# Kernel optimization log

Hardware: AMD Instinct MI355X
Metric: run time of the kernel (lower is better)

The kernel has to match this reference:

```python
import jax, jax.numpy as jnp
import numpy as np

C_M, C_Z, H, C_HID = 256, 128, 8, 32
N_SEQ, N_RES = 64, 384
INF = 1e9
EPS = 1e-5


def layernorm(x, w, b):
    mu = jnp.mean(x, axis=-1, keepdims=True)
    var = jnp.mean(jnp.square(x - mu), axis=-1, keepdims=True)
    return (x - mu) * jax.lax.rsqrt(var + EPS) * w + b


def setup_inputs() -> dict:
    key = jax.random.key(0)
    ks = jax.random.split(key, 6)
    m = jax.random.normal(ks[0], (N_SEQ, N_RES, C_M), dtype=jnp.float32)
    z = jax.random.normal(ks[1], (N_RES, N_RES, C_Z), dtype=jnp.float32)
    mask = jnp.ones((N_SEQ, N_RES), dtype=jnp.float32)
    return {
        "m": m,
        "z": z,
        "mask": mask,
        "ln_m_w": jnp.ones((C_M,), jnp.float32),
        "ln_m_b": jnp.zeros((C_M,), jnp.float32),
        "ln_z_w": jnp.ones((C_Z,), jnp.float32),
        "ln_z_b": jnp.zeros((C_Z,), jnp.float32),
        "W_z": jax.random.normal(ks[2], (C_Z, H), jnp.float32) * 0.05,
        "W_v": jax.random.normal(ks[3], (C_M, H * C_HID), jnp.float32) * 0.05,
        "W_g": jax.random.normal(ks[4], (C_M, H * C_HID), jnp.float32) * 0.05,
        "W_o": jax.random.normal(ks[5], (H * C_HID, C_M), jnp.float32) * 0.05,
    }


def reference(m, z, mask, ln_m_w, ln_m_b, ln_z_w, ln_z_b, W_z, W_v, W_g, W_o):
    S, N = m.shape[0], m.shape[1]
    # mask: max over MSA rows, keepdim -> [1, N]; bias -> [1,1,1,N]
    mask_max = jnp.max(mask, axis=-2, keepdims=True)
    mask_bias = (INF * (mask_max - 1.0))[:, None, None, :]  # [1,1,1,N]
    # pair bias: LN(z) @ W_z -> [N,N,H] -> [H,N,N]
    zb = layernorm(z, ln_z_w, ln_z_b) @ W_z  # [N,N,H]
    zb = jnp.transpose(zb, (2, 0, 1))  # [H,N,N]
    # LN on m
    m_ln = layernorm(m, ln_m_w, ln_m_b)  # [S,N,C_m]
    # values: [S,N,H*c] -> [S,H,N,c]
    v = (m_ln @ W_v).reshape(S, N, H, C_HID).transpose(0, 2, 1, 3)
    # attention weights from summed biases (no QK): [1,H,N,N] after broadcast
    a = jax.nn.softmax(mask_bias + zb[None], axis=-1)  # [1,H,N,N]
    # o = a @ v  -> [S,H,N,c]
    o = jnp.einsum('hqk,shkc->shqc', a[0], v)
    o = o.transpose(0, 2, 1, 3)  # [S,N,H,c]
    # sigmoid gate
    g = jax.nn.sigmoid(m_ln @ W_g).reshape(S, N, H, C_HID)
    o = (o * g).reshape(S, N, H * C_HID)
    return o @ W_o  # [S,N,C_m]
```

## Files before the change

### kernel.cpp

```cpp
#include <hip/hip_runtime.h>
#include <math.h>

#define S 64
#define NRES 384
#define CM 256
#define CZ 128
#define NH 8
#define CH 32
#define HC 256
#define NROW 147456

typedef unsigned short u16;
typedef __attribute__((ext_vector_type(8))) short bf16x8;
typedef __attribute__((ext_vector_type(4))) float f32x4;
typedef __attribute__((ext_vector_type(8))) unsigned short ushort8;
typedef __attribute__((ext_vector_type(4))) unsigned short ushort4_t;

#define OFF_BIAS 0
#define OFF_WWT  8192
#define OFF_C1   16384
#define OFF_C2   16448
#define OFF_WT   200704
#define OFF_WOT  462848
#define OFF_A    593920
#define OFF_VT   2953216
#define OFF_G    15536128
#define OFF_O    28119040
#define OFF_MLN  40701952
#define OFF_ZB   OFF_O

__device__ __forceinline__ u16 f2bf(float f) {
    union { float f; unsigned int u; } v; v.f = f;
    unsigned int u = v.u;
    u += 0x7fff + ((u >> 16) & 1);
    return (u16)(u >> 16);
}
__device__ __forceinline__ float bf2f(u16 b) {
    union { float f; unsigned int u; } v; v.u = ((unsigned int)b) << 16;
    return v.f;
}
__device__ __forceinline__ void gload16(const u16* g, u16* l) {
    __builtin_amdgcn_global_load_lds(
        (const __attribute__((address_space(1))) void*)g,
        (__attribute__((address_space(3))) void*)l, 16, 0, 0);
}

__global__ __launch_bounds__(256) void k_pre(
        const float* __restrict__ mask, const float* __restrict__ Wz,
        const float* __restrict__ lzw, const float* __restrict__ lzb,
        const float* __restrict__ Wv, const float* __restrict__ Wg,
        const float* __restrict__ Wo, const float* __restrict__ m,
        const float* __restrict__ lmw, const float* __restrict__ lmb,
        float* __restrict__ bias, u16* __restrict__ WWT,
        float* __restrict__ C1, float* __restrict__ C2,
        u16* __restrict__ Wt, u16* __restrict__ Wot, u16* __restrict__ mln) {
    __shared__ float sRed[4][64];
    const int bid = blockIdx.x, tid = threadIdx.x;
    const int wave = tid >> 6, lane = tid & 63;
    if (bid < 6) {
        const int k = bid * 64 + lane;
        float mx = -1e30f;
        #pragma unroll
        for (int i = 0; i < 16; ++i) {
            const int s = wave * 16 + i;
            mx = fmaxf(mx, mask[(size_t)s * NRES + k]);
        }
        sRed[wave][lane] = mx;
        __syncthreads();
        if (wave == 0) {
            mx = fmaxf(fmaxf(sRed[0][lane], sRed[1][lane]),
                       fmaxf(sRed[2][lane], sRed[3][lane]));
            bias[k] = 1e9f * (mx - 1.0f);
        }
    } else if (bid == 6) {
        __shared__ float sP[2][2][8];
        if (tid < 128) {
            const int c = tid;
            const float4 wz0 = *(const float4*)&Wz[c * 8];
            const float4 wz1 = *(const float4*)&Wz[c * 8 + 4];
            const float lw = lzw[c], lbv = lzb[c];
            float wzv[8] = {wz0.x, wz0.y, wz0.z, wz0.w, wz1.x, wz1.y, wz1.z, wz1.w};
            float ww[8], wb[8];
            #pragma unroll
            for (int h = 0; h < 8; ++h) {
                ww[h] = lw * wzv[h];
                wb[h] = lbv * wzv[h];
                WWT[h * 128 + c] = f2bf(ww[h]);
                WWT[(8 + h) * 128 + c] = 0;
            }
            #pragma unroll
            for (int h = 0; h < 8; ++h) {
                #pragma unroll
                for (int off = 1; off < 64; off <<= 1) {
                    ww[h] += __shfl_xor(ww[h], off);
                    wb[h] += __shfl_xor(wb[h], off);
                }
            }
            if (lane == 0) {
                #pragma unroll
                for (int h = 0; h < 8; ++h) {
                    sP[wave][0][h] = ww[h];
                    sP[wave][1][h] = wb[h];
                }
            }
        }
        __syncthreads();
        if (tid < 8) {
            C1[tid] = sP[0][0][tid] + sP[1][0][tid];
            C2[tid] = sP[0][1][tid] + sP[1][1][tid];
        }
    } else if (bid < 519) {
        const int i = (bid - 7) * 256 + tid;
        const int n = i >> 8, k = i & 255;
        const float v = (n < HC) ? Wv[(size_t)k * HC + n] : Wg[(size_t)k * HC + (n - HC)];
        Wt[i] = f2bf(v);
    } else if (bid < 775) {
        const int i = (bid - 519) * 256 + tid;
        const int n = i >> 8, k = i & 255;
        Wot[i] = f2bf(Wo[(size_t)k * CM + n]);
    } else {
        const int row = (bid - 775) * 4 + wave;
        const float4 x = *(const float4*)&m[(size_t)row * CM + lane * 4];
        float sm = x.x + x.y + x.z + x.w;
        float sq = x.x*x.x + x.y*x.y + x.z*x.z + x.w*x.w;
        #pragma unroll
        for (int off = 32; off >= 1; off >>= 1) {
            sm += __shfl_xor(sm, off);
            sq += __shfl_xor(sq, off);
        }
        const float mu = sm * (1.0f / CM);
        const float var = sq * (1.0f / CM) - mu * mu;
        const float rs = rsqrtf(var + 1e-5f);
        const float4 w4 = *(const float4*)&lmw[lane * 4];
        const float4 b4 = *(const float4*)&lmb[lane * 4];
        u16 t4[4];
        t4[0] = f2bf((x.x - mu) * rs * w4.x + b4.x);
        t4[1] = f2bf((x.y - mu) * rs * w4.y + b4.y);
        t4[2] = f2bf((x.z - mu) * rs * w4.z + b4.z);
        t4[3] = f2bf((x.w - mu) * rs * w4.w + b4.w);
        *(ushort4_t*)&mln[(size_t)row * CM + lane * 4] = *(ushort4_t*)t4;
    }
}

__global__ __launch_bounds__(256) void k_zb(
        const float* __restrict__ z, const u16* __restrict__ WWT,
        const float* __restrict__ C1, const float* __restrict__ C2,
        float* __restrict__ zb) {
    __shared__ u16 sZ[4][2048];
    __shared__ float sSt[4][2][16];
    const int tid = threadIdx.x, wave = tid >> 6, lane = tid & 63;
    const int rl = lane & 15, kg = lane >> 4;
    u16* myZ = &sZ[wave][0];
    const int row0 = blockIdx.x * 64 + wave * 16;
    const float4* zbase = (const float4*)(z + (size_t)row0 * CZ);
    float4 xb[8];
    #pragma unroll
    for (int j = 0; j < 8; ++j) xb[j] = zbase[lane + 64 * j];
    bf16x8 bfr[4];
    #pragma unroll
    for (int t = 0; t < 4; ++t)
        bfr[t] = *(const bf16x8*)&WWT[rl * 128 + t * 32 + kg * 8];
    const float c1 = (rl < 8) ? C1[rl] : 0.f;
    const float c2 = (rl < 8) ? C2[rl] : 0.f;
    const int hw = lane >> 5, c4 = lane & 31;
    float smj[8], sqj[8];
    #pragma unroll
    for (int j = 0; j < 8; ++j) {
        const int r = 2 * j + hw;
        const float4 x = xb[j];
        float xs[4] = {x.x, x.y, x.z, x.w};
        float sm = 0.f, sq = 0.f;
        u16 t4[4];
        #pragma unroll
        for (int e = 0; e < 4; ++e) {
            sm += xs[e]; sq += xs[e] * xs[e];
            t4[e] = f2bf(xs[e]);
        }
        smj[j] = sm; sqj[j] = sq;
        *(ushort4_t*)&myZ[r * 128 + ((c4 >> 1) ^ (r & 7)) * 8 + (c4 & 1) * 4] =
            *(ushort4_t*)t4;
    }
    #pragma unroll
    for (int j = 0; j < 8; ++j) {
        #pragma unroll
        for (int off = 1; off < 32; off <<= 1) {
            smj[j] += __shfl_xor(smj[j], off);
            sqj[j] += __shfl_xor(sqj[j], off);
        }
    }
    if ((lane & 31) == 0) {
        #pragma unroll
        for (int j = 0; j < 8; ++j) {
            const int r = 2 * j + hw;
            const float mu = smj[j] * (1.0f / CZ);
            const float var = sqj[j] * (1.0f / CZ) - mu * mu;
            sSt[wave][0][r] = mu;
            sSt[wave][1][r] = rsqrtf(var + 1e-5f);
        }
    }
    bf16x8 af[4];
    #pragma unroll
    for (int t = 0; t < 4; ++t)
        af[t] = *(const bf16x8*)&myZ[rl * 128 + ((t * 4 + kg) ^ (rl & 7)) * 8];
    f32x4 acc = {};
    #pragma unroll
    for (int t = 0; t < 4; ++t)
        acc = __builtin_amdgcn_mfma_f32_16x16x32_bf16(af[t], bfr[t], acc, 0, 0, 0);
    f32x4 pv;
    #pragma unroll
    for (int r = 0; r < 4; ++r) {
        const int rr = kg * 4 + r;
        pv[r] = sSt[wave][1][rr] * (acc[r] - sSt[wave][0][rr] * c1) + c2;
    }
    if (rl < 8)
        *(f32x4*)&zb[(size_t)rl * NROW + row0 + kg * 4] = pv;
}

__global__ __launch_bounds__(256) void k_stage2(
        const u16* __restrict__ mln, const u16* __restrict__ Wt,
        const float* __restrict__ zb, const float* __restrict__ bias,
        u16* __restrict__ vt, u16* __restrict__ g_, u16* __restrict__ a_out) {
    __shared__ u16 As[128][32];
    __shared__ u16 Bs[128][32];
    const int bid = blockIdx.x, tid = threadIdx.x;
    if (bid >= 768) {
        const int w = (bid - 768) * 4 + (tid >> 6);
        const int lane = tid & 63;
        const int h = w & 7, q = w >> 3;
        const float* zbh = zb + (size_t)h * NROW + (size_t)q * NRES;
        float v[6];
        float mx = -1e30f;
        #pragma unroll
        for (int t = 0; t < 6; ++t) {
            const int k = lane + 64 * t;
            v[t] = zbh[k] + bias[k];
            mx = fmaxf(mx, v[t]);
        }
        #pragma unroll
        for (int off = 32; off >= 1; off >>= 1) mx = fmaxf(mx, __shfl_xor(mx, off));
        float sum = 0.f;
        #pragma unroll
        for (int t = 0; t < 6; ++t) { v[t] = expf(v[t] - mx); sum += v[t]; }
        #pragma unroll
        for (int off = 32; off >= 1; off >>= 1) sum += __shfl_xor(sum, off);
        const float inv = 1.0f / sum;
        #pragma unroll
        for (int t = 0; t < 6; ++t)
            a_out[((size_t)h * NRES + q) * NRES + lane + 64 * t] = f2bf(v[t] * inv);
        return;
    }
    const int xcd = bid & 7, idx = bid >> 3;
    const int nt = idx & 3, mt = xcd * 24 + (idx >> 2);
    const int m0 = mt * 128, n0 = nt * 128;
    const int wave = tid >> 6, lane = tid & 63;
    const int wm = (wave >> 1) * 64, wn = (wave & 1) * 64;
    const int rl = lane & 15, kg = lane >> 4;
    const int lr = lane >> 2, lk = (lane & 3) * 8;
    const int wr = wave * 32;
    const u16* ag  = mln + (size_t)(m0 + wr + lr) * CM + lk;
    const u16* ag2 = ag + 16 * CM;
    const u16* bg  = Wt + (size_t)(n0 + wr + lr) * CM + lk;
    const u16* bg2 = bg + 16 * CM;
    u16* al  = &As[wr][0];
    u16* al2 = &As[wr + 16][0];
    u16* bl  = &Bs[wr][0];
    u16* bl2 = &Bs[wr + 16][0];
    const bool vhalf = (n0 < HC);
    f32x4 acc[4][4] = {};
    for (int kt = 0; kt < CM; kt += 32) {
        if (kt) __syncthreads();
        gload16(ag + kt, al);  gload16(ag2 + kt, al2);
        gload16(bg + kt, bl);  gload16(bg2 + kt, bl2);
        __syncthreads();
        bf16x8 af[4], bfr[4];
        #pragma unroll
        for (int i = 0; i < 4; ++i) af[i]  = *(const bf16x8*)&As[wm + i*16 + rl][kg*8];
        #pragma unroll
        for (int j = 0; j < 4; ++j) bfr[j] = *(const bf16x8*)&Bs[wn + j*16 + rl][kg*8];
        if (vhalf) {
            #pragma unroll
            for (int j = 0; j < 4; ++j)
                #pragma unroll
                for (int i = 0; i < 4; ++i)
                    acc[j][i] = __builtin_amdgcn_mfma_f32_16x16x32_bf16(bfr[j], af[i], acc[j][i], 0, 0, 0);
        } else {
            #pragma unroll
            for (int i = 0; i < 4; ++i)
                #pragma unroll
                for (int j = 0; j < 4; ++j)
                    acc[i][j] = __builtin_amdgcn_mfma_f32_16x16x32_bf16(af[i], bfr[j], acc[i][j], 0, 0, 0);
        }
    }
    if (vhalf) {
        #pragma unroll
        for (int j = 0; j < 4; ++j)
            #pragma unroll
            for (int r = 0; r < 4; ++r) {
                const int vcol = n0 + wn + j*16 + kg*4 + r;
                const int h = vcol >> 5, c = vcol & 31;
                #pragma unroll
                for (int i = 0; i < 4; ++i) {
                    const int mrowb = m0 + wm + i*16;
                    const int s = mrowb / NRES;
                    const int nn = mrowb - s * NRES + rl;
                    vt[(((size_t)h * S + s) * CH + c) * NRES + nn] = f2bf(acc[j][i][r]);
                }
            }
    } else {
        #pragma unroll
        for (int i = 0; i < 4; ++i)
            #pragma unroll
            for (int r = 0; r < 4; ++r) {
                const int row = m0 + wm + i*16 + kg*4 + r;
                #pragma unroll
                for (int j = 0; j < 4; ++j) {
                    const int gc = n0 + wn + j*16 + rl - HC;
                    g_[(size_t)row * HC + gc] = f2bf(1.0f / (1.0f + expf(-acc[i][j][r])));
                }
            }
    }
}

__global__ __launch_bounds__(256) void k_attn2(const u16* __restrict__ a_,
        const u16* __restrict__ vt, u16* __restrict__ o_) {
    __shared__ u16 As[128][32];
    __shared__ u16 Bs[128][32];
    const int tid = threadIdx.x;
    const int h = blockIdx.x & 7, rem = blockIdx.x >> 3;
    const int mt = rem >> 4, nt = rem & 15;
    const int q0 = mt * 128, sc0 = nt * 128;
    const int wave = tid >> 6, lane = tid & 63;
    const int wm = (wave >> 1) * 64, wn = (wave & 1) * 64;
    const int rl = lane & 15, kg = lane >> 4;
    const int lr = lane >> 2, lk = (lane & 3) * 8;
    const int wr = wave * 32;
    const u16* ag  = a_ + (size_t)h * NRES * NRES + (size_t)(q0 + wr + lr) * NRES + lk;
    const u16* ag2 = ag + 16 * NRES;
    const u16* bg  = vt + (size_t)h * S * CH * NRES + (size_t)(sc0 + wr + lr) * NRES + lk;
    const u16* bg2 = bg + 16 * NRES;
    u16* al  = &As[wr][0];
    u16* al2 = &As[wr + 16][0];
    u16* bl  = &Bs[wr][0];
    u16* bl2 = &Bs[wr + 16][0];
    f32x4 acc[4][4] = {};
    for (int kt = 0; kt < NRES; kt += 32) {
        if (kt) __syncthreads();
        gload16(ag + kt, al);  gload16(ag2 + kt, al2);
        gload16(bg + kt, bl);  gload16(bg2 + kt, bl2);
        __syncthreads();
        bf16x8 af[4], bfr[4];
        #pragma unroll
        for (int i = 0; i < 4; ++i) af[i]  = *(const bf16x8*)&As[wm + i*16 + rl][kg*8];
        #pragma unroll
        for (int j = 0; j < 4; ++j) bfr[j] = *(const bf16x8*)&Bs[wn + j*16 + rl][kg*8];
        #pragma unroll
        for (int i = 0; i < 4; ++i)
            #pragma unroll
            for (int j = 0; j < 4; ++j)
                acc[i][j] = __builtin_amdgcn_mfma_f32_16x16x32_bf16(af[i], bfr[j], acc[i][j], 0, 0, 0);
    }
    #pragma unroll
    for (int i = 0; i < 4; ++i)
        #pragma unroll
        for (int r = 0; r < 4; ++r) {
            const int q = q0 + wm + i*16 + kg*4 + r;
            #pragma unroll
            for (int j = 0; j < 4; ++j) {
                const int sc = sc0 + wn + j*16 + rl;
                const int s = sc >> 5, c = sc & 31;
                o_[(((size_t)s * NRES + q) * NH + h) * CH + c] = f2bf(acc[i][j][r]);
            }
        }
}

__global__ __launch_bounds__(256) void k_gemm_out(const u16* __restrict__ o_,
        const u16* __restrict__ g_, const u16* __restrict__ Wot,
        float* __restrict__ out) {
    __shared__ u16 As[128][40];
    __shared__ u16 Bs[128][32];
    const int tid = threadIdx.x;
    const int xcd = blockIdx.x & 7, idx = blockIdx.x >> 3;
    const int nt = idx & 1, mt = xcd * 24 + (idx >> 1);
    const int m0 = mt * 128, n0 = nt * 128;
    const int wave = tid >> 6, lane = tid & 63;
    const int wm = (wave >> 1) * 64, wn = (wave & 1) * 64;
    const int rl = lane & 15, kg = lane >> 4;
    const int lr = lane >> 2, lk = (lane & 3) * 8;
    const int wr = wave * 32;
    const int sr = tid >> 1, sh = (tid & 1) * 16;
    const u16* orow = o_ + (size_t)(m0 + sr) * HC;
    const u16* grow = g_ + (size_t)(m0 + sr) * HC;
    const u16* bg  = Wot + (size_t)(n0 + wr + lr) * HC + lk;
    const u16* bg2 = bg + 16 * HC;
    u16* bl  = &Bs[wr][0];
    u16* bl2 = &Bs[wr + 16][0];
    f32x4 acc[4][4] = {};
    for (int kt = 0; kt < HC; kt += 32) {
        if (kt) __syncthreads();
        gload16(bg + kt, bl);  gload16(bg2 + kt, bl2);
        {
            u16 tmp[16];
            const ushort8 ov0 = *(const ushort8*)&orow[kt + sh];
            const ushort8 ov1 = *(const ushort8*)&orow[kt + sh + 8];
            const ushort8 gv0 = *(const ushort8*)&grow[kt + sh];
            const ushort8 gv1 = *(const ushort8*)&grow[kt + sh + 8];
            #pragma unroll
            for (int p = 0; p < 8; ++p) {
                tmp[p]     = f2bf(bf2f(ov0[p]) * bf2f(gv0[p]));
                tmp[p + 8] = f2bf(bf2f(ov1[p]) * bf2f(gv1[p]));
            }
            *(ushort8*)&As[sr][sh]     = *(ushort8*)&tmp[0];
            *(ushort8*)&As[sr][sh + 8] = *(ushort8*)&tmp[8];
        }
        __syncthreads();
        bf16x8 af[4], bfr[4];
        #pragma unroll
        for (int i = 0; i < 4; ++i) af[i]  = *(const bf16x8*)&As[wm + i*16 + rl][kg*8];
        #pragma unroll
        for (int j = 0; j < 4; ++j) bfr[j] = *(const bf16x8*)&Bs[wn + j*16 + rl][kg*8];
        #pragma unroll
        for (int i = 0; i < 4; ++i)
            #pragma unroll
            for (int j = 0; j < 4; ++j)
                acc[i][j] = __builtin_amdgcn_mfma_f32_16x16x32_bf16(af[i], bfr[j], acc[i][j], 0, 0, 0);
    }
    #pragma unroll
    for (int i = 0; i < 4; ++i)
        #pragma unroll
        for (int r = 0; r < 4; ++r) {
            const int row = m0 + wm + i*16 + kg*4 + r;
            #pragma unroll
            for (int j = 0; j < 4; ++j)
                out[(size_t)row * CM + n0 + wn + j*16 + rl] = acc[i][j][r];
        }
}

extern "C" void kernel_launch(void* const* d_in, const int* in_sizes, int n_in,
                              void* d_out, int out_size, void* d_ws, size_t ws_size,
                              hipStream_t stream) {
    const float* m      = (const float*)d_in[0];
    const float* z      = (const float*)d_in[1];
    const float* mask   = (const float*)d_in[2];
    const float* ln_m_w = (const float*)d_in[3];
    const float* ln_m_b = (const float*)d_in[4];
    const float* ln_z_w = (const float*)d_in[5];
    const float* ln_z_b = (const float*)d_in[6];
    const float* Wz     = (const float*)d_in[7];
    const float* Wv     = (const float*)d_in[8];
    const float* Wg     = (const float*)d_in[9];
    const float* Wo     = (const float*)d_in[10];
    float* out = (float*)d_out;
    char* ws = (char*)d_ws;

    float* bias = (float*)(ws + OFF_BIAS);
    u16* WWT    = (u16*)(ws + OFF_WWT);
    float* C1   = (float*)(ws + OFF_C1);
    float* C2   = (float*)(ws + OFF_C2);
    u16* Wt     = (u16*)(ws + OFF_WT);
    u16* Wot    = (u16*)(ws + OFF_WOT);
    u16* a      = (u16*)(ws + OFF_A);
    u16* vtw    = (u16*)(ws + OFF_VT);
    u16* gw     = (u16*)(ws + OFF_G);
    u16* ow     = (u16*)(ws + OFF_O);
    u16* mlnw   = (u16*)(ws + OFF_MLN);
    float* zbw  = (float*)(ws + OFF_ZB);

    k_pre<<<6919, 256, 0, stream>>>(mask, Wz, ln_z_w, ln_z_b, Wv, Wg, Wo, m,
                                    ln_m_w, ln_m_b, bias, WWT, C1, C2, Wt, Wot, mlnw);
    k_zb<<<2304, 256, 0, stream>>>(z, WWT, C1, C2, zbw);
    k_stage2<<<1536, 256, 0, stream>>>(mlnw, Wt, zbw, bias, vtw, gw, a);
    k_attn2<<<384, 256, 0, stream>>>(a, vtw, ow);
    k_gemm_out<<<384, 256, 0, stream>>>(ow, gw, Wot, out);
}
```

Before: 76.59 us.

## Fuse z-bias projection with V/G GEMM in one launch, split softmax out

The pair-bias LayerNorm+projection blocks and the V/gate GEMM blocks now share one grid, interleaved 24:8 per group of 32 blocks. The memory-bound z stream can then overlap with the MFMA-heavy GEMM. Softmax moves into its own small kernel after that. Kernel count stays the same. Shared memory is unified to a single buffer, which may affect occupancy.

```diff
diff --git a/kernel.cpp b/kernel.cpp
--- a/kernel.cpp
+++ b/kernel.cpp
@@ -142,129 +142,105 @@
     }
 }
 
-__global__ __launch_bounds__(256) void k_zb(
+__global__ __launch_bounds__(256) void k_mid(
         const float* __restrict__ z, const u16* __restrict__ WWT,
         const float* __restrict__ C1, const float* __restrict__ C2,
-        float* __restrict__ zb) {
-    __shared__ u16 sZ[4][2048];
-    __shared__ float sSt[4][2][16];
-    const int tid = threadIdx.x, wave = tid >> 6, lane = tid & 63;
+        const u16* __restrict__ mln, const u16* __restrict__ Wt,
+        float* __restrict__ zb, u16* __restrict__ vt, u16* __restrict__ g_) {
+    __shared__ u16 SM[8704];
+    const int bid = blockIdx.x, tid = threadIdx.x;
+    const int wave = tid >> 6, lane = tid & 63;
     const int rl = lane & 15, kg = lane >> 4;
-    u16* myZ = &sZ[wave][0];
-    const int row0 = blockIdx.x * 64 + wave * 16;
-    const float4* zbase = (const float4*)(z + (size_t)row0 * CZ);
-    float4 xb[8];
-    #pragma unroll
-    for (int j = 0; j < 8; ++j) xb[j] = zbase[lane + 64 * j];
-    bf16x8 bfr[4];
-    #pragma unroll
-    for (int t = 0; t < 4; ++t)
-        bfr[t] = *(const bf16x8*)&WWT[rl * 128 + t * 32 + kg * 8];
-    const float c1 = (rl < 8) ? C1[rl] : 0.f;
-    const float c2 = (rl < 8) ? C2[rl] : 0.f;
-    const int hw = lane >> 5, c4 = lane & 31;
-    float smj[8], sqj[8];
-    #pragma unroll
-    for (int j = 0; j < 8; ++j) {
-        const int r = 2 * j + hw;
-        const float4 x = xb[j];
-        float xs[4] = {x.x, x.y, x.z, x.w};
-        float sm = 0.f, sq = 0.f;
-        u16 t4[4];
-        #pragma unroll
-        for (int e = 0; e < 4; ++e) {
-            sm += xs[e]; sq += xs[e] * xs[e];
-            t4[e] = f2bf(xs[e]);
-        }
-        smj[j] = sm; sqj[j] = sq;
-        *(ushort4_t*)&myZ[r * 128 + ((c4 >> 1) ^ (r & 7)) * 8 + (c4 & 1) * 4] =
-            *(ushort4_t*)t4;
-    }
-    #pragma unroll
-    for (int j = 0; j < 8; ++j) {
-        #pragma unroll
-        for (int off = 1; off < 32; off <<= 1) {
-            smj[j] += __shfl_xor(smj[j], off);
-            sqj[j] += __shfl_xor(sqj[j], off);
-        }
-    }
-    if ((lane & 31) == 0) {
+    const int sub = bid & 31;
+
+    if (sub < 24) {
+        const int zbid = (bid >> 5) * 24 + sub;
+        u16* myZ = SM + wave * 2048;
+        float* sSt = (float*)(SM + 8192);
+        const int row0 = zbid * 64 + wave * 16;
+        const float4* zbase = (const float4*)(z + (size_t)row0 * CZ);
+        float4 xb[8];
+        #pragma unroll
+        for (int j = 0; j < 8; ++j) xb[j] = zbase[lane + 64 * j];
+        bf16x8 bfr[4];
+        #pragma unroll
+        for (int t = 0; t < 4; ++t)
+            bfr[t] = *(const bf16x8*)&WWT[rl * 128 + t * 32 + kg * 8];
+        const float c1 = (rl < 8) ? C1[rl] : 0.f;
+        const float c2 = (rl < 8) ? C2[rl] : 0.f;
+        const int hw = lane >> 5, c4 = lane & 31;
+        float smj[8], sqj[8];
         #pragma unroll
         for (int j = 0; j < 8; ++j) {
             const int r = 2 * j + hw;
-            const float mu = smj[j] * (1.0f / CZ);
-            const float var = sqj[j] * (1.0f / CZ) - mu * mu;
-            sSt[wave][0][r] = mu;
-            sSt[wave][1][r] = rsqrtf(var + 1e-5f);
-        }
-    }
-    bf16x8 af[4];
-    #pragma unroll
-    for (int t = 0; t < 4; ++t)
-        af[t] = *(const bf16x8*)&myZ[rl * 128 + ((t * 4 + kg) ^ (rl & 7)) * 8];
-    f32x4 acc = {};
-    #pragma unroll
-    for (int t = 0; t < 4; ++t)
-        acc = __builtin_amdgcn_mfma_f32_16x16x32_bf16(af[t], bfr[t], acc, 0, 0, 0);
-    f32x4 pv;
-    #pragma unroll
-    for (int r = 0; r < 4; ++r) {
-        const int rr = kg * 4 + r;
-        pv[r] = sSt[wave][1][rr] * (acc[r] - sSt[wave][0][rr] * c1) + c2;
-    }
-    if (rl < 8)
-        *(f32x4*)&zb[(size_t)rl * NROW + row0 + kg * 4] = pv;
-}
-
-__global__ __launch_bounds__(256) void k_stage2(
-        const u16* __restrict__ mln, const u16* __restrict__ Wt,
-        const float* __restrict__ zb, const float* __restrict__ bias,
-        u16* __restrict__ vt, u16* __restrict__ g_, u16* __restrict__ a_out) {
-    __shared__ u16 As[128][32];
-    __shared__ u16 Bs[128][32];
-    const int bid = blockIdx.x, tid = threadIdx.x;
-    if (bid >= 768) {
-        const int w = (bid - 768) * 4 + (tid >> 6);
-        const int lane = tid & 63;
-        const int h = w & 7, q = w >> 3;
-        const float* zbh = zb + (size_t)h * NROW + (size_t)q * NRES;
-        float v[6];
-        float mx = -1e30f;
-        #pragma unroll
-        for (int t = 0; t < 6; ++t) {
-            const int k = lane + 64 * t;
-            v[t] = zbh[k] + bias[k];
-            mx = fmaxf(mx, v[t]);
-        }
-        #pragma unroll
-        for (int off = 32; off >= 1; off >>= 1) mx = fmaxf(mx, __shfl_xor(mx, off));
-        float sum = 0.f;
-        #pragma unroll
-        for (int t = 0; t < 6; ++t) { v[t] = expf(v[t] - mx); sum += v[t]; }
-        #pragma unroll
-        for (int off = 32; off >= 1; off >>= 1) sum += __shfl_xor(sum, off);
-        const float inv = 1.0f / sum;
-        #pragma unroll
-        for (int t = 0; t < 6; ++t)
-            a_out[((size_t)h * NRES + q) * NRES + lane + 64 * t] = f2bf(v[t] * inv);
+            const float4 x = xb[j];
+            float xs[4] = {x.x, x.y, x.z, x.w};
+            float sm = 0.f, sq = 0.f;
+            u16 t4[4];
+            #pragma unroll
+            for (int e = 0; e < 4; ++e) {
+                sm += xs[e]; sq += xs[e] * xs[e];
+                t4[e] = f2bf(xs[e]);
+            }
+            smj[j] = sm; sqj[j] = sq;
+            *(ushort4_t*)&myZ[r * 128 + ((c4 >> 1) ^ (r & 7)) * 8 + (c4 & 1) * 4] =
+                *(ushort4_t*)t4;
+        }
+        #pragma unroll
+        for (int j = 0; j < 8; ++j) {
+            #pragma unroll
+            for (int off = 1; off < 32; off <<= 1) {
+                smj[j] += __shfl_xor(smj[j], off);
+                sqj[j] += __shfl_xor(sqj[j], off);
+            }
+        }
+        if ((lane & 31) == 0) {
+            #pragma unroll
+            for (int j = 0; j < 8; ++j) {
+                const int r = 2 * j + hw;
+                const float mu = smj[j] * (1.0f / CZ);
+                const float var = sqj[j] * (1.0f / CZ) - mu * mu;
+                sSt[(wave * 2 + 0) * 16 + r] = mu;
+                sSt[(wave * 2 + 1) * 16 + r] = rsqrtf(var + 1e-5f);
+            }
+        }
+        bf16x8 af[4];
+        #pragma unroll
+        for (int t = 0; t < 4; ++t)
+            af[t] = *(const bf16x8*)&myZ[rl * 128 + ((t * 4 + kg) ^ (rl & 7)) * 8];
+        f32x4 acc = {};
+        #pragma unroll
+        for (int t = 0; t < 4; ++t)
+            acc = __builtin_amdgcn_mfma_f32_16x16x32_bf16(af[t], bfr[t], acc, 0, 0, 0);
+        f32x4 pv;
+        #pragma unroll
+        for (int r = 0; r < 4; ++r) {
+            const int rr = kg * 4 + r;
+            pv[r] = sSt[(wave * 2 + 1) * 16 + rr] *
+                    (acc[r] - sSt[(wave * 2 + 0) * 16 + rr] * c1) + c2;
+        }
+        if (rl < 8)
+            *(f32x4*)&zb[(size_t)rl * NROW + row0 + kg * 4] = pv;
         return;
     }
-    const int xcd = bid & 7, idx = bid >> 3;
+
+    const int vgid = (bid >> 5) * 8 + (sub - 24);
+    const int xcd = vgid & 7, idx = vgid >> 3;
     const int nt = idx & 3, mt = xcd * 24 + (idx >> 2);
     const int m0 = mt * 128, n0 = nt * 128;
-    const int wave = tid >> 6, lane = tid & 63;
     const int wm = (wave >> 1) * 64, wn = (wave & 1) * 64;
-    const int rl = lane & 15, kg = lane >> 4;
     const int lr = lane >> 2, lk = (lane & 3) * 8;
     const int wr = wave * 32;
+    u16* As = SM;
+    u16* Bs = SM + 4096;
     const u16* ag  = mln + (size_t)(m0 + wr + lr) * CM + lk;
     const u16* ag2 = ag + 16 * CM;
     const u16* bg  = Wt + (size_t)(n0 + wr + lr) * CM + lk;
     const u16* bg2 = bg + 16 * CM;
-    u16* al  = &As[wr][0];
-    u16* al2 = &As[wr + 16][0];
-    u16* bl  = &Bs[wr][0];
-    u16* bl2 = &Bs[wr + 16][0];
+    u16* al  = As + wr * 32;
+    u16* al2 = As + (wr + 16) * 32;
+    u16* bl  = Bs + wr * 32;
+    u16* bl2 = Bs + (wr + 16) * 32;
     const bool vhalf = (n0 < HC);
     f32x4 acc[4][4] = {};
     for (int kt = 0; kt < CM; kt += 32) {
@@ -274,9 +250,9 @@
         __syncthreads();
         bf16x8 af[4], bfr[4];
         #pragma unroll
-        for (int i = 0; i < 4; ++i) af[i]  = *(const bf16x8*)&As[wm + i*16 + rl][kg*8];
-        #pragma unroll
-        for (int j = 0; j < 4; ++j) bfr[j] = *(const bf16x8*)&Bs[wn + j*16 + rl][kg*8];
+        for (int i = 0; i < 4; ++i) af[i]  = *(const bf16x8*)&As[(wm + i*16 + rl) * 32 + kg*8];
+        #pragma unroll
+        for (int j = 0; j < 4; ++j) bfr[j] = *(const bf16x8*)&Bs[(wn + j*16 + rl) * 32 + kg*8];
         if (vhalf) {
             #pragma unroll
             for (int j = 0; j < 4; ++j)
@@ -319,6 +295,34 @@
                 }
             }
     }
+}
+
+__global__ __launch_bounds__(256) void k_soft(
+        const float* __restrict__ zb, const float* __restrict__ bias,
+        u16* __restrict__ a_out) {
+    const int w = blockIdx.x * 4 + (threadIdx.x >> 6);
+    const int lane = threadIdx.x & 63;
+    const int h = w & 7, q = w >> 3;
+    const float* zbh = zb + (size_t)h * NROW + (size_t)q * NRES;
+    float v[6];
+    float mx = -1e30f;
+    #pragma unroll
+    for (int t = 0; t < 6; ++t) {
+        const int k = lane + 64 * t;
+        v[t] = zbh[k] + bias[k];
+        mx = fmaxf(mx, v[t]);
+    }
+    #pragma unroll
+    for (int off = 32; off >= 1; off >>= 1) mx = fmaxf(mx, __shfl_xor(mx, off));
+    float sum = 0.f;
+    #pragma unroll
+    for (int t = 0; t < 6; ++t) { v[t] = expf(v[t] - mx); sum += v[t]; }
+    #pragma unroll
+    for (int off = 32; off >= 1; off >>= 1) sum += __shfl_xor(sum, off);
+    const float inv = 1.0f / sum;
+    #pragma unroll
+    for (int t = 0; t < 6; ++t)
+        a_out[((size_t)h * NRES + q) * NRES + lane + 64 * t] = f2bf(v[t] * inv);
 }
 
 __global__ __launch_bounds__(256) void k_attn2(const u16* __restrict__ a_,
@@ -467,8 +471,8 @@
 
     k_pre<<<6919, 256, 0, stream>>>(mask, Wz, ln_z_w, ln_z_b, Wv, Wg, Wo, m,
                                     ln_m_w, ln_m_b, bias, WWT, C1, C2, Wt, Wot, mlnw);
-    k_zb<<<2304, 256, 0, stream>>>(z, WWT, C1, C2, zbw);
-    k_stage2<<<1536, 256, 0, stream>>>(mlnw, Wt, zbw, bias, vtw, gw, a);
+    k_mid<<<3072, 256, 0, stream>>>(z, WWT, C1, C2, mlnw, Wt, zbw, vtw, gw);
+    k_soft<<<768, 256, 0, stream>>>(zbw, bias, a);
     k_attn2<<<384, 256, 0, stream>>>(a, vtw, ow);
     k_gemm_out<<<384, 256, 0, stream>>>(ow, gw, Wot, out);
 }
```

New measurement: 99.59 us. 30.0% more time.
